# Kernel tuning notes

Measured on AMD Instinct MI355X. Metric: run time of the kernel, lower is better.

The kernel has to match this reference:

```python
import jax, jax.numpy as jnp
import numpy as np


def setup_inputs() -> dict:
    key = jax.random.key(0)
    N, D = 131072, 128
    x = jax.random.normal(key, (N, D), dtype=jnp.float32)
    return {"x": x, "k": 1024, "niters": 10}


def reference(x, k, niters):
    """Lloyd's k-means, Euclidean metric. Returns (clusters, centroids, n_points).

    Matches torch semantics: clusters are the assignments computed at the START
    of the last iteration (against the previous centroids); centroids/n_points
    reflect the update performed in that last iteration. Empty clusters divide
    by zero (-> inf/nan), same as the torch code.
    """
    K = int(k)
    x_sq = jnp.sum(x * x, axis=-1)  # [N], constant across iterations
    c0 = x[:K]

    def step(centroids, _):
        d = (x_sq[:, None]
             - 2.0 * jnp.einsum('nd,kd->nk', x, centroids)
             + jnp.sum(centroids * centroids, axis=-1)[None, :])
        clusters = jnp.argmin(d, axis=1)  # [N] int32
        sums = jax.ops.segment_sum(x, clusters, num_segments=K)  # [K, D] scatter-add
        counts = jax.ops.segment_sum(jnp.ones((x.shape[0],), x.dtype), clusters,
                                     num_segments=K)  # [K] bincount
        new_centroids = sums / counts[:, None]
        return new_centroids, (clusters, counts)

    centroids, (clusters_hist, counts_hist) = jax.lax.scan(step, c0, None, length=int(niters))
    return clusters_hist[-1].astype(jnp.int64), centroids, counts_hist[-1]
```

## Files before the change

kernel.cpp:

```cpp
#include <hip/hip_runtime.h>
#include <math.h>

#define DIM 128
#define KC 1024
#define NITER 10
#define BM 128
#define NB 512
#define THRESH 0.01f

typedef __bf16 bf16x8 __attribute__((ext_vector_type(8)));
typedef float f32x4 __attribute__((ext_vector_type(4)));

__device__ __forceinline__ unsigned short bf16rne(float f) {
    unsigned int u = __float_as_uint(f);
    unsigned int r = (u + 0x7FFFu + ((u >> 16) & 1u)) >> 16;
    return (unsigned short)r;
}

__device__ __forceinline__ bf16x8 pack_hi8(const float* fv, unsigned short* hs) {
    bf16x8 out;
    #pragma unroll
    for (int e = 0; e < 8; e++) {
        unsigned short h = bf16rne(fv[e]);
        hs[e] = h;
        out[e] = __builtin_bit_cast(__bf16, h);
    }
    return out;
}

__global__ void sq_np_kernel(const float* __restrict__ v, float* __restrict__ out, int rows) {
    int i = blockIdx.x * blockDim.x + threadIdx.x;
    if (i >= rows) return;
    const float4* row = (const float4*)(v + (size_t)i * DIM);
    float r[8];
    {
        float4 a = row[0], b = row[1];
        r[0] = __fmul_rn(a.x, a.x); r[1] = __fmul_rn(a.y, a.y);
        r[2] = __fmul_rn(a.z, a.z); r[3] = __fmul_rn(a.w, a.w);
        r[4] = __fmul_rn(b.x, b.x); r[5] = __fmul_rn(b.y, b.y);
        r[6] = __fmul_rn(b.z, b.z); r[7] = __fmul_rn(b.w, b.w);
    }
    #pragma unroll
    for (int blk = 1; blk < 16; blk++) {
        float4 a = row[blk * 2], b = row[blk * 2 + 1];
        r[0] = __fadd_rn(r[0], __fmul_rn(a.x, a.x));
        r[1] = __fadd_rn(r[1], __fmul_rn(a.y, a.y));
        r[2] = __fadd_rn(r[2], __fmul_rn(a.z, a.z));
        r[3] = __fadd_rn(r[3], __fmul_rn(a.w, a.w));
        r[4] = __fadd_rn(r[4], __fmul_rn(b.x, b.x));
        r[5] = __fadd_rn(r[5], __fmul_rn(b.y, b.y));
        r[6] = __fadd_rn(r[6], __fmul_rn(b.z, b.z));
        r[7] = __fadd_rn(r[7], __fmul_rn(b.w, b.w));
    }
    out[i] = __fadd_rn(__fadd_rn(__fadd_rn(r[0], r[1]), __fadd_rn(r[2], r[3])),
                       __fadd_rn(__fadd_rn(r[4], r[5]), __fadd_rn(r[6], r[7])));
}

__global__ __launch_bounds__(256, 3) void assign_mfma_kernel(
    const float* __restrict__ x,
    const ushort* __restrict__ centPh, const ushort* __restrict__ centPl,
    const float* __restrict__ csq,
    int* __restrict__ cl, int* __restrict__ fb_list, int* __restrict__ fbc)
{
    const int tid = threadIdx.x;
    const int lane = tid & 63;
    const int w = tid >> 6;
    const int bm = blockIdx.x * BM;
    const int row0 = bm + w * 32 + (lane & 15);
    const int ko = (lane >> 4) * 8;

    bf16x8 ah[2][4], al[2][4];
    #pragma unroll
    for (int m = 0; m < 2; m++) {
        const float* xr = x + (size_t)(row0 + m * 16) * DIM;
        #pragma unroll
        for (int dt = 0; dt < 4; dt++) {
            float4 a = *(const float4*)(xr + dt * 32 + ko);
            float4 b = *(const float4*)(xr + dt * 32 + ko + 4);
            float fv[8] = {a.x, a.y, a.z, a.w, b.x, b.y, b.z, b.w};
            unsigned short hs[8];
            ah[m][dt] = pack_hi8(fv, hs);
            bf16x8 lo;
            #pragma unroll
            for (int e = 0; e < 8; e++) {
                float rem = __fsub_rn(fv[e], __uint_as_float(((unsigned int)hs[e]) << 16));
                lo[e] = __builtin_bit_cast(__bf16, bf16rne(rem));
            }
            al[m][dt] = lo;
        }
    }

    float best1[8], best2[8];
    int bidx[8];
    int nanf = 0;
    #pragma unroll
    for (int s = 0; s < 8; s++) { best1[s] = INFINITY; best2[s] = INFINITY; bidx[s] = 0; }

    const ushort* pb = centPh + lane * 8;
    const ushort* qb = centPl + lane * 8;
    int kk = lane & 15;

    for (int kt = 0; kt < KC / 16; kt++) {
        const ushort* pk = pb + (size_t)kt * 2048;
        const ushort* qk = qb + (size_t)kt * 2048;
        bf16x8 bh0 = *(const bf16x8*)(pk);
        bf16x8 bh1 = *(const bf16x8*)(pk + 512);
        bf16x8 bh2 = *(const bf16x8*)(pk + 1024);
        bf16x8 bh3 = *(const bf16x8*)(pk + 1536);
        bf16x8 bl0 = *(const bf16x8*)(qk);
        bf16x8 bl1 = *(const bf16x8*)(qk + 512);
        bf16x8 bl2 = *(const bf16x8*)(qk + 1024);
        bf16x8 bl3 = *(const bf16x8*)(qk + 1536);

        f32x4 a0 = (f32x4){0.f, 0.f, 0.f, 0.f};
        f32x4 a1 = (f32x4){0.f, 0.f, 0.f, 0.f};
#define DT(BH, BL, D)                                                      \
        a0 = __builtin_amdgcn_mfma_f32_16x16x32_bf16(ah[0][D], BH, a0, 0, 0, 0); \
        a1 = __builtin_amdgcn_mfma_f32_16x16x32_bf16(ah[1][D], BH, a1, 0, 0, 0); \
        a0 = __builtin_amdgcn_mfma_f32_16x16x32_bf16(ah[0][D], BL, a0, 0, 0, 0); \
        a1 = __builtin_amdgcn_mfma_f32_16x16x32_bf16(ah[1][D], BL, a1, 0, 0, 0); \
        a0 = __builtin_amdgcn_mfma_f32_16x16x32_bf16(al[0][D], BH, a0, 0, 0, 0); \
        a1 = __builtin_amdgcn_mfma_f32_16x16x32_bf16(al[1][D], BH, a1, 0, 0, 0);
        DT(bh0, bl0, 0)
        DT(bh1, bl1, 1)
        DT(bh2, bl2, 2)
        DT(bh3, bl3, 3)
#undef DT

        float cq = csq[kk];
        nanf |= (cq != cq) ? 1 : 0;
        #pragma unroll
        for (int q = 0; q < 4; q++) {
            {
                float d = __fmaf_rn(-2.f, a0[q], cq);
                bool lt = (d < best1[q]);
                best2[q] = fminf(best2[q], lt ? best1[q] : d);
                if (lt) { best1[q] = d; bidx[q] = kk; }
            }
            {
                int s = 4 + q;
                float d = __fmaf_rn(-2.f, a1[q], cq);
                bool lt = (d < best1[s]);
                best2[s] = fminf(best2[s], lt ? best1[s] : d);
                if (lt) { best1[s] = d; bidx[s] = kk; }
            }
        }
        kk += 16;
    }

    #pragma unroll
    for (int mask = 1; mask < 16; mask <<= 1) {
        #pragma unroll
        for (int s = 0; s < 8; s++) {
            float ob1 = __shfl_xor(best1[s], mask, 64);
            float ob2 = __shfl_xor(best2[s], mask, 64);
            int   oi  = __shfl_xor(bidx[s],  mask, 64);
            float nb2 = fminf(fminf(best2[s], ob2), fmaxf(best1[s], ob1));
            bool take = (ob1 < best1[s]) || (ob1 == best1[s] && oi < bidx[s]);
            if (take) { best1[s] = ob1; bidx[s] = oi; }
            best2[s] = nb2;
        }
    }

    int wnan = __any(nanf);
    if ((lane & 15) == 0) {
        int hi = lane >> 4;
        #pragma unroll
        for (int s = 0; s < 8; s++) {
            int p = bm + w * 32 + (s >> 2) * 16 + hi * 4 + (s & 3);
            bool fb = (wnan != 0) || !(best2[s] - best1[s] > THRESH);
            if (fb) { int pos = atomicAdd(fbc, 1); fb_list[pos] = p; }
            else cl[p] = bidx[s];
        }
    }
}

__device__ __forceinline__ bool better(float od, int oi, float md, int mi) {
    bool n1 = (md != md), n2 = (od != od);
    if (n1 && n2) return oi < mi;
    if (n2) return true;
    if (n1) return false;
    return (od < md) || (od == md && oi < mi);
}

__global__ __launch_bounds__(256) void fixup_kernel(
    const float* __restrict__ x, const float* __restrict__ centTf,
    const float* __restrict__ xsq, const float* __restrict__ csq,
    const int* __restrict__ fb_list, const int* __restrict__ fbc,
    int* __restrict__ cl)
{
    __shared__ float xs[4][DIM];
    __shared__ float sv[256];
    __shared__ int si[256];
    const int t = threadIdx.x;
    const int cnt = fbc[0];
    for (int w = blockIdx.x * 4; w < cnt; w += gridDim.x * 4) {
        int np = cnt - w; if (np > 4) np = 4;
        __syncthreads();
        for (int e = t; e < np * DIM; e += 256) {
            int p = e >> 7, d = e & 127;
            xs[p][d] = x[(size_t)fb_list[w + p] * DIM + d];
        }
        __syncthreads();
        float S[4][4];
        #pragma unroll
        for (int p = 0; p < 4; p++)
            #pragma unroll
            for (int c = 0; c < 4; c++) S[p][c] = 0.f;
        for (int d = 0; d < DIM; d++) {
            const float* row = centTf + (size_t)d * KC;
            float c0 = row[t], c1 = row[t + 256], c2 = row[t + 512], c3 = row[t + 768];
            #pragma unroll
            for (int p = 0; p < 4; p++) {
                float xv = xs[p][d];
                S[p][0] = fmaf(xv, c0, S[p][0]);
                S[p][1] = fmaf(xv, c1, S[p][1]);
                S[p][2] = fmaf(xv, c2, S[p][2]);
                S[p][3] = fmaf(xv, c3, S[p][3]);
            }
        }
        #pragma unroll
        for (int p = 0; p < 4; p++) {
            if (p < np) {
                int i = fb_list[w + p];
                float xq = xsq[i];
                float bb = INFINITY; int bi = 0x7fffffff;
                float dd; int c;
                c = t;       dd = __fadd_rn(__fsub_rn(xq, __fmul_rn(2.f, S[p][0])), csq[c]); if (better(dd, c, bb, bi)) { bb = dd; bi = c; }
                c = t + 256; dd = __fadd_rn(__fsub_rn(xq, __fmul_rn(2.f, S[p][1])), csq[c]); if (better(dd, c, bb, bi)) { bb = dd; bi = c; }
                c = t + 512; dd = __fadd_rn(__fsub_rn(xq, __fmul_rn(2.f, S[p][2])), csq[c]); if (better(dd, c, bb, bi)) { bb = dd; bi = c; }
                c = t + 768; dd = __fadd_rn(__fsub_rn(xq, __fmul_rn(2.f, S[p][3])), csq[c]); if (better(dd, c, bb, bi)) { bb = dd; bi = c; }
                sv[t] = bb; si[t] = bi;
                __syncthreads();
                for (int o = 128; o > 0; o >>= 1) {
                    if (t < o) {
                        if (better(sv[t + o], si[t + o], sv[t], si[t])) { sv[t] = sv[t + o]; si[t] = si[t + o]; }
                    }
                    __syncthreads();
                }
                if (t == 0) cl[i] = si[0];
                __syncthreads();
            }
        }
    }
}


__global__ __launch_bounds__(256) void bhist_kernel(const int* __restrict__ cl,
                                                    int* __restrict__ bhist, int n) {
    __shared__ int h[KC];
    int t = threadIdx.x;
    #pragma unroll
    for (int q = 0; q < KC / 256; q++) h[t + q * 256] = 0;
    __syncthreads();
    int i = blockIdx.x * 256 + t;
    if (i < n) atomicAdd(&h[cl[i]], 1);
    __syncthreads();
    int* row = bhist + (size_t)blockIdx.x * KC;
    #pragma unroll
    for (int q = 0; q < KC / 256; q++) row[t + q * 256] = h[t + q * 256];
}

__global__ __launch_bounds__(256) void colsum_kernel(const int* __restrict__ bhist,
                                                     int* __restrict__ cnt) {
    int k = blockIdx.x * 256 + threadIdx.x;
    int s = 0;
    for (int b = 0; b < NB; b++) s += bhist[(size_t)b * KC + k];
    cnt[k] = s;
}

__global__ void scan_kernel(const int* __restrict__ cnt, int* __restrict__ off) {
    __shared__ int s[KC];
    int t = threadIdx.x;
    s[t] = cnt[t];
    __syncthreads();
    for (int o = 1; o < KC; o <<= 1) {
        int v = (t >= o) ? s[t - o] : 0;
        __syncthreads();
        s[t] += v;
        __syncthreads();
    }
    off[t] = s[t] - cnt[t];
}

__global__ __launch_bounds__(256) void blockpfx_kernel(int* __restrict__ bhist,
                                                       const int* __restrict__ off) {
    int k = blockIdx.x * 256 + threadIdx.x;
    int run = off[k];
    for (int b = 0; b < NB; b++) {
        size_t idx = (size_t)b * KC + k;
        int t = bhist[idx];
        bhist[idx] = run;
        run += t;
    }
}

__global__ __launch_bounds__(256) void stable_scatter_kernel(
    const int* __restrict__ cl, const int* __restrict__ bhist,
    int* __restrict__ list, int n)
{
    __shared__ int cls[256];
    int t = threadIdx.x;
    int i = blockIdx.x * 256 + t;
    int c = (i < n) ? cl[i] : -1;
    cls[t] = c;
    __syncthreads();
    if (i >= n) return;
    int rank = 0;
    for (int j = 0; j < 256; j++)
        rank += (j < t && cls[j] == c) ? 1 : 0;
    list[bhist[(size_t)blockIdx.x * KC + c] + rank] = i;
}

#define CHUNK 512
__global__ __launch_bounds__(128) void sum_kernel(
    const float* __restrict__ x, const int* __restrict__ list,
    const int* __restrict__ off, const int* __restrict__ cnt,
    float* __restrict__ cent, ushort* __restrict__ centPh,
    ushort* __restrict__ centPl, float* __restrict__ centTf,
    float* __restrict__ countsF)
{
    __shared__ int sidx[CHUNK];
    int k = blockIdx.x;
    int d = threadIdx.x;
    int o = off[k], m = cnt[k];
    float s = 0.f;
    for (int base = 0; base < m; base += CHUNK) {
        int c = m - base; if (c > CHUNK) c = CHUNK;
        __syncthreads();
        for (int t = d; t < c; t += 128) sidx[t] = list[o + base + t];
        __syncthreads();
        int j = 0;
        for (; j + 16 <= c; j += 16) {
            float v[16];
            #pragma unroll
            for (int u = 0; u < 16; u++)
                v[u] = x[(size_t)sidx[j + u] * DIM + d];
            #pragma unroll
            for (int u = 0; u < 16; u++)
                s = __fadd_rn(s, v[u]);
        }
        for (; j < c; j++)
            s = __fadd_rn(s, x[(size_t)sidx[j] * DIM + d]);
    }
    float mv = __fdiv_rn(s, (float)m);
    cent[(size_t)k * DIM + d] = mv;
    centTf[(size_t)d * KC + k] = mv;
    unsigned short h = bf16rne(mv);
    unsigned short lo = bf16rne(__fsub_rn(mv, __uint_as_float(((unsigned int)h) << 16)));
    int pidx = (((k >> 4) * 4 + (d >> 5)) * 64 + ((k & 15) + 16 * ((d >> 3) & 3))) * 8 + (d & 7);
    centPh[pidx] = h;
    centPl[pidx] = lo;
    if (d == 0) countsF[k] = (float)m;
}

__global__ void init_centP_kernel(const float* __restrict__ x,
                                  ushort* __restrict__ centPh, ushort* __restrict__ centPl,
                                  float* __restrict__ centTf) {
    int i = blockIdx.x * 256 + threadIdx.x;
    if (i < KC * DIM) {
        int k = i >> 7, d = i & 127;
        float v = x[i];
        centTf[(size_t)d * KC + k] = v;
        unsigned short h = bf16rne(v);
        unsigned short lo = bf16rne(__fsub_rn(v, __uint_as_float(((unsigned int)h) << 16)));
        int pidx = (((k >> 4) * 4 + (d >> 5)) * 64 + ((k & 15) + 16 * ((d >> 3) & 3))) * 8 + (d & 7);
        centPh[pidx] = h;
        centPl[pidx] = lo;
    }
}

__global__ void cl2f_kernel(const int* __restrict__ cl, float* __restrict__ out, int n) {
    int i = blockIdx.x * 256 + threadIdx.x;
    if (i < n) out[i] = (float)cl[i];
}

extern "C" void kernel_launch(void* const* d_in, const int* in_sizes, int n_in,
                              void* d_out, int out_size, void* d_ws, size_t ws_size,
                              hipStream_t stream) {
    const float* x = (const float*)d_in[0];
    const int n = in_sizes[0] / DIM;

    float* clf     = (float*)d_out;
    float* cent    = clf + n;
    float* countsF = cent + KC * DIM;

    float* xsq   = (float*)d_ws;
    float* csq   = xsq + n;
    int*   cl    = (int*)(csq + KC);
    int*   list  = cl + n;
    int*   cnt   = list + n;
    int*   off   = cnt + KC;
    int*   bhist = off + KC;
    ushort* centPh = (ushort*)(bhist + (size_t)NB * KC);
    ushort* centPl = centPh + KC * DIM;
    int*   fbc   = (int*)(centPl + KC * DIM);
    float* centTf = (float*)bhist;

    hipMemcpyAsync(cent, x, (size_t)KC * DIM * sizeof(float),
                   hipMemcpyDeviceToDevice, stream);
    init_centP_kernel<<<(KC * DIM + 255) / 256, 256, 0, stream>>>(x, centPh, centPl, centTf);
    sq_np_kernel<<<(n + 255) / 256, 256, 0, stream>>>(x, xsq, n);

    for (int it = 0; it < NITER; it++) {
        sq_np_kernel<<<(KC + 255) / 256, 256, 0, stream>>>(cent, csq, KC);
        hipMemsetAsync(fbc, 0, 2 * sizeof(int), stream);
        assign_mfma_kernel<<<n / BM, 256, 0, stream>>>(x, centPh, centPl, csq,
                                                       cl, list, fbc);
        fixup_kernel<<<1024, 256, 0, stream>>>(x, centTf, xsq, csq, list, fbc, cl);
        bhist_kernel<<<NB, 256, 0, stream>>>(cl, bhist, n);
        colsum_kernel<<<KC / 256, 256, 0, stream>>>(bhist, cnt);
        scan_kernel<<<1, KC, 0, stream>>>(cnt, off);
        blockpfx_kernel<<<KC / 256, 256, 0, stream>>>(bhist, off);
        stable_scatter_kernel<<<NB, 256, 0, stream>>>(cl, bhist, list, n);
        sum_kernel<<<KC, DIM, 0, stream>>>(x, list, off, cnt, cent, centPh, centPl, centTf, countsF);
    }

    cl2f_kernel<<<(n + 255) / 256, 256, 0, stream>>>(cl, clf, n);
}
```

Before: 2.142 ms.

## Switch split-precision MFMA from bf16 to fp16 and batch fixup rescoring

Replaces the bf16 hi/lo split used for the distance GEMM with an fp16 hi/lo split, which keeps more mantissa bits. Because the MFMA distances are more accurate, the ambiguity threshold for exact fp32 rescoring drops, so fewer points go to the fallback path. The fixup kernel now handles 16 points per block and reduces with wave shuffles instead of a per-point shared-memory tree with many barriers. The argmin update is also made branchless. fp16 has a narrower exponent range than bf16, which could overflow or lose precision for inputs with a wider dynamic range than the test data.

```diff
diff --git a/kernel.cpp b/kernel.cpp
--- a/kernel.cpp
+++ b/kernel.cpp
@@ -6,27 +6,10 @@
 #define NITER 10
 #define BM 128
 #define NB 512
-#define THRESH 0.01f
-
-typedef __bf16 bf16x8 __attribute__((ext_vector_type(8)));
+#define THRESH 0.004f
+
+typedef _Float16 f16x8 __attribute__((ext_vector_type(8)));
 typedef float f32x4 __attribute__((ext_vector_type(4)));
-
-__device__ __forceinline__ unsigned short bf16rne(float f) {
-    unsigned int u = __float_as_uint(f);
-    unsigned int r = (u + 0x7FFFu + ((u >> 16) & 1u)) >> 16;
-    return (unsigned short)r;
-}
-
-__device__ __forceinline__ bf16x8 pack_hi8(const float* fv, unsigned short* hs) {
-    bf16x8 out;
-    #pragma unroll
-    for (int e = 0; e < 8; e++) {
-        unsigned short h = bf16rne(fv[e]);
-        hs[e] = h;
-        out[e] = __builtin_bit_cast(__bf16, h);
-    }
-    return out;
-}
 
 __global__ void sq_np_kernel(const float* __restrict__ v, float* __restrict__ out, int rows) {
     int i = blockIdx.x * blockDim.x + threadIdx.x;
@@ -69,7 +52,7 @@
     const int row0 = bm + w * 32 + (lane & 15);
     const int ko = (lane >> 4) * 8;
 
-    bf16x8 ah[2][4], al[2][4];
+    f16x8 ah[2][4], al[2][4];
     #pragma unroll
     for (int m = 0; m < 2; m++) {
         const float* xr = x + (size_t)(row0 + m * 16) * DIM;
@@ -78,15 +61,12 @@
             float4 a = *(const float4*)(xr + dt * 32 + ko);
             float4 b = *(const float4*)(xr + dt * 32 + ko + 4);
             float fv[8] = {a.x, a.y, a.z, a.w, b.x, b.y, b.z, b.w};
-            unsigned short hs[8];
-            ah[m][dt] = pack_hi8(fv, hs);
-            bf16x8 lo;
             #pragma unroll
             for (int e = 0; e < 8; e++) {
-                float rem = __fsub_rn(fv[e], __uint_as_float(((unsigned int)hs[e]) << 16));
-                lo[e] = __builtin_bit_cast(__bf16, bf16rne(rem));
+                _Float16 h = (_Float16)fv[e];
+                ah[m][dt][e] = h;
+                al[m][dt][e] = (_Float16)__fsub_rn(fv[e], (float)h);
             }
-            al[m][dt] = lo;
         }
     }
 
@@ -103,24 +83,24 @@
     for (int kt = 0; kt < KC / 16; kt++) {
         const ushort* pk = pb + (size_t)kt * 2048;
         const ushort* qk = qb + (size_t)kt * 2048;
-        bf16x8 bh0 = *(const bf16x8*)(pk);
-        bf16x8 bh1 = *(const bf16x8*)(pk + 512);
-        bf16x8 bh2 = *(const bf16x8*)(pk + 1024);
-        bf16x8 bh3 = *(const bf16x8*)(pk + 1536);
-        bf16x8 bl0 = *(const bf16x8*)(qk);
-        bf16x8 bl1 = *(const bf16x8*)(qk + 512);
-        bf16x8 bl2 = *(const bf16x8*)(qk + 1024);
-        bf16x8 bl3 = *(const bf16x8*)(qk + 1536);
+        f16x8 bh0 = *(const f16x8*)(pk);
+        f16x8 bh1 = *(const f16x8*)(pk + 512);
+        f16x8 bh2 = *(const f16x8*)(pk + 1024);
+        f16x8 bh3 = *(const f16x8*)(pk + 1536);
+        f16x8 bl0 = *(const f16x8*)(qk);
+        f16x8 bl1 = *(const f16x8*)(qk + 512);
+        f16x8 bl2 = *(const f16x8*)(qk + 1024);
+        f16x8 bl3 = *(const f16x8*)(qk + 1536);
 
         f32x4 a0 = (f32x4){0.f, 0.f, 0.f, 0.f};
         f32x4 a1 = (f32x4){0.f, 0.f, 0.f, 0.f};
 #define DT(BH, BL, D)                                                      \
-        a0 = __builtin_amdgcn_mfma_f32_16x16x32_bf16(ah[0][D], BH, a0, 0, 0, 0); \
-        a1 = __builtin_amdgcn_mfma_f32_16x16x32_bf16(ah[1][D], BH, a1, 0, 0, 0); \
-        a0 = __builtin_amdgcn_mfma_f32_16x16x32_bf16(ah[0][D], BL, a0, 0, 0, 0); \
-        a1 = __builtin_amdgcn_mfma_f32_16x16x32_bf16(ah[1][D], BL, a1, 0, 0, 0); \
-        a0 = __builtin_amdgcn_mfma_f32_16x16x32_bf16(al[0][D], BH, a0, 0, 0, 0); \
-        a1 = __builtin_amdgcn_mfma_f32_16x16x32_bf16(al[1][D], BH, a1, 0, 0, 0);
+        a0 = __builtin_amdgcn_mfma_f32_16x16x32_f16(ah[0][D], BH, a0, 0, 0, 0); \
+        a1 = __builtin_amdgcn_mfma_f32_16x16x32_f16(ah[1][D], BH, a1, 0, 0, 0); \
+        a0 = __builtin_amdgcn_mfma_f32_16x16x32_f16(ah[0][D], BL, a0, 0, 0, 0); \
+        a1 = __builtin_amdgcn_mfma_f32_16x16x32_f16(ah[1][D], BL, a1, 0, 0, 0); \
+        a0 = __builtin_amdgcn_mfma_f32_16x16x32_f16(al[0][D], BH, a0, 0, 0, 0); \
+        a1 = __builtin_amdgcn_mfma_f32_16x16x32_f16(al[1][D], BH, a1, 0, 0, 0);
         DT(bh0, bl0, 0)
         DT(bh1, bl1, 1)
         DT(bh2, bl2, 2)
@@ -133,16 +113,18 @@
         for (int q = 0; q < 4; q++) {
             {
                 float d = __fmaf_rn(-2.f, a0[q], cq);
+                best2[q] = fminf(best2[q], fmaxf(best1[q], d));
                 bool lt = (d < best1[q]);
-                best2[q] = fminf(best2[q], lt ? best1[q] : d);
-                if (lt) { best1[q] = d; bidx[q] = kk; }
+                best1[q] = fminf(best1[q], d);
+                bidx[q] = lt ? kk : bidx[q];
             }
             {
                 int s = 4 + q;
                 float d = __fmaf_rn(-2.f, a1[q], cq);
+                best2[s] = fminf(best2[s], fmaxf(best1[s], d));
                 bool lt = (d < best1[s]);
-                best2[s] = fminf(best2[s], lt ? best1[s] : d);
-                if (lt) { best1[s] = d; bidx[s] = kk; }
+                best1[s] = fminf(best1[s], d);
+                bidx[s] = lt ? kk : bidx[s];
             }
         }
         kk += 16;
@@ -189,29 +171,34 @@
     const int* __restrict__ fb_list, const int* __restrict__ fbc,
     int* __restrict__ cl)
 {
-    __shared__ float xs[4][DIM];
-    __shared__ float sv[256];
-    __shared__ int si[256];
+    __shared__ float xs[16][DIM];
+    __shared__ float xqs[16];
+    __shared__ int   ids[16];
+    __shared__ float wv[16][4];
+    __shared__ int   wi[16][4];
     const int t = threadIdx.x;
+    const int lane = t & 63, wid = t >> 6;
     const int cnt = fbc[0];
-    for (int w = blockIdx.x * 4; w < cnt; w += gridDim.x * 4) {
-        int np = cnt - w; if (np > 4) np = 4;
+    for (int w = blockIdx.x * 16; w < cnt; w += gridDim.x * 16) {
+        int np = cnt - w; if (np > 16) np = 16;
+        __syncthreads();
+        if (t < np) { int i = fb_list[w + t]; ids[t] = i; xqs[t] = xsq[i]; }
         __syncthreads();
         for (int e = t; e < np * DIM; e += 256) {
             int p = e >> 7, d = e & 127;
-            xs[p][d] = x[(size_t)fb_list[w + p] * DIM + d];
-        }
-        __syncthreads();
-        float S[4][4];
-        #pragma unroll
-        for (int p = 0; p < 4; p++)
+            xs[p][d] = x[(size_t)ids[p] * DIM + d];
+        }
+        __syncthreads();
+        float S[16][4];
+        #pragma unroll
+        for (int p = 0; p < 16; p++)
             #pragma unroll
             for (int c = 0; c < 4; c++) S[p][c] = 0.f;
         for (int d = 0; d < DIM; d++) {
             const float* row = centTf + (size_t)d * KC;
             float c0 = row[t], c1 = row[t + 256], c2 = row[t + 512], c3 = row[t + 768];
             #pragma unroll
-            for (int p = 0; p < 4; p++) {
+            for (int p = 0; p < 16; p++) {
                 float xv = xs[p][d];
                 S[p][0] = fmaf(xv, c0, S[p][0]);
                 S[p][1] = fmaf(xv, c1, S[p][1]);
@@ -219,28 +206,31 @@
                 S[p][3] = fmaf(xv, c3, S[p][3]);
             }
         }
-        #pragma unroll
-        for (int p = 0; p < 4; p++) {
-            if (p < np) {
-                int i = fb_list[w + p];
-                float xq = xsq[i];
-                float bb = INFINITY; int bi = 0x7fffffff;
-                float dd; int c;
-                c = t;       dd = __fadd_rn(__fsub_rn(xq, __fmul_rn(2.f, S[p][0])), csq[c]); if (better(dd, c, bb, bi)) { bb = dd; bi = c; }
-                c = t + 256; dd = __fadd_rn(__fsub_rn(xq, __fmul_rn(2.f, S[p][1])), csq[c]); if (better(dd, c, bb, bi)) { bb = dd; bi = c; }
-                c = t + 512; dd = __fadd_rn(__fsub_rn(xq, __fmul_rn(2.f, S[p][2])), csq[c]); if (better(dd, c, bb, bi)) { bb = dd; bi = c; }
-                c = t + 768; dd = __fadd_rn(__fsub_rn(xq, __fmul_rn(2.f, S[p][3])), csq[c]); if (better(dd, c, bb, bi)) { bb = dd; bi = c; }
-                sv[t] = bb; si[t] = bi;
-                __syncthreads();
-                for (int o = 128; o > 0; o >>= 1) {
-                    if (t < o) {
-                        if (better(sv[t + o], si[t + o], sv[t], si[t])) { sv[t] = sv[t + o]; si[t] = si[t + o]; }
-                    }
-                    __syncthreads();
-                }
-                if (t == 0) cl[i] = si[0];
-                __syncthreads();
+        float q0 = csq[t], q1 = csq[t + 256], q2 = csq[t + 512], q3 = csq[t + 768];
+        #pragma unroll
+        for (int p = 0; p < 16; p++) {
+            float xq = xqs[p];
+            float bb = INFINITY; int bi = 0x7fffffff;
+            float dd; int c;
+            c = t;       dd = __fadd_rn(__fsub_rn(xq, __fmul_rn(2.f, S[p][0])), q0); if (better(dd, c, bb, bi)) { bb = dd; bi = c; }
+            c = t + 256; dd = __fadd_rn(__fsub_rn(xq, __fmul_rn(2.f, S[p][1])), q1); if (better(dd, c, bb, bi)) { bb = dd; bi = c; }
+            c = t + 512; dd = __fadd_rn(__fsub_rn(xq, __fmul_rn(2.f, S[p][2])), q2); if (better(dd, c, bb, bi)) { bb = dd; bi = c; }
+            c = t + 768; dd = __fadd_rn(__fsub_rn(xq, __fmul_rn(2.f, S[p][3])), q3); if (better(dd, c, bb, bi)) { bb = dd; bi = c; }
+            #pragma unroll
+            for (int mask = 1; mask < 64; mask <<= 1) {
+                float od = __shfl_xor(bb, mask, 64);
+                int   oi = __shfl_xor(bi, mask, 64);
+                if (better(od, oi, bb, bi)) { bb = od; bi = oi; }
             }
+            if (lane == 0) { wv[p][wid] = bb; wi[p][wid] = bi; }
+        }
+        __syncthreads();
+        if (t < np) {
+            float bb = wv[t][0]; int bi = wi[t][0];
+            #pragma unroll
+            for (int r = 1; r < 4; r++)
+                if (better(wv[t][r], wi[t][r], bb, bi)) { bb = wv[t][r]; bi = wi[t][r]; }
+            cl[ids[t]] = bi;
         }
     }
 }
@@ -346,11 +336,11 @@
     float mv = __fdiv_rn(s, (float)m);
     cent[(size_t)k * DIM + d] = mv;
     centTf[(size_t)d * KC + k] = mv;
-    unsigned short h = bf16rne(mv);
-    unsigned short lo = bf16rne(__fsub_rn(mv, __uint_as_float(((unsigned int)h) << 16)));
+    _Float16 h = (_Float16)mv;
+    float rem = __fsub_rn(mv, (float)h);
     int pidx = (((k >> 4) * 4 + (d >> 5)) * 64 + ((k & 15) + 16 * ((d >> 3) & 3))) * 8 + (d & 7);
-    centPh[pidx] = h;
-    centPl[pidx] = lo;
+    centPh[pidx] = __builtin_bit_cast(unsigned short, h);
+    centPl[pidx] = __builtin_bit_cast(unsigned short, (_Float16)rem);
     if (d == 0) countsF[k] = (float)m;
 }
 
@@ -362,11 +352,11 @@
         int k = i >> 7, d = i & 127;
         float v = x[i];
         centTf[(size_t)d * KC + k] = v;
-        unsigned short h = bf16rne(v);
-        unsigned short lo = bf16rne(__fsub_rn(v, __uint_as_float(((unsigned int)h) << 16)));
+        _Float16 h = (_Float16)v;
+        float rem = __fsub_rn(v, (float)h);
         int pidx = (((k >> 4) * 4 + (d >> 5)) * 64 + ((k & 15) + 16 * ((d >> 3) & 3))) * 8 + (d & 7);
-        centPh[pidx] = h;
-        centPl[pidx] = lo;
+        centPh[pidx] = __builtin_bit_cast(unsigned short, h);
+        centPl[pidx] = __builtin_bit_cast(unsigned short, (_Float16)rem);
     }
 }
 
```

After: 3.206 ms. +49.7%, slower.
